# Kernel optimization log

Hardware: AMD Instinct MI355X
Metric: run time of the kernel (lower is better)

Reference implementation:

```python
import jax, jax.numpy as jnp
import numpy as np

B, I, H = 32768, 512, 512


def _uniform(key, shape, fan_in):
    bound = 1.0 / np.sqrt(fan_in)
    return jax.random.uniform(key, shape, jnp.float32, -bound, bound)


def setup_inputs() -> dict:
    key = jax.random.key(0)
    ks = jax.random.split(key, 16)
    inp = {
        "x": jax.random.normal(ks[0], (B, I), jnp.float32),
        "h": jax.random.normal(ks[1], (B, H), jnp.float32),
        "c_prev": jax.random.normal(ks[2], (B, H), jnp.float32),
        # weights stored as [in, out] so we apply x @ W (transpose of torch layout)
        "Wxi": _uniform(ks[3], (I, H), I), "bxi": _uniform(ks[4], (H,), I),
        "Whi": _uniform(ks[5], (H, H), H),
        "Wxf": _uniform(ks[6], (I, H), I), "bxf": _uniform(ks[7], (H,), I),
        "Whf": _uniform(ks[8], (H, H), H),
        "Wxc": _uniform(ks[9], (I, H), I), "bxc": _uniform(ks[10], (H,), I),
        "Whc": _uniform(ks[11], (H, H), H),
        "Wxo": _uniform(ks[12], (I, H), I), "bxo": _uniform(ks[13], (H,), I),
        "Who": _uniform(ks[14], (H, H), H),
    }
    return inp


def reference(x, h, c_prev, Wxi, bxi, Whi, Wxf, bxf, Whf, Wxc, bxc, Whc, Wxo, bxo, Who):
    # Faithful to source: peephole (w_c) projections are dead code; the
    # forget path f*c_prev is computed then discarded, so c_next = i * tanh(.)
    i = jax.nn.sigmoid(x @ Wxi + bxi + h @ Whi)            # input gate
    f = jax.nn.sigmoid(x @ Wxf + bxf + h @ Whf)            # computed, unused (as in source)
    c_next = i * jnp.tanh(x @ Wxc + bxc + h @ Whc)         # NOTE: no f*c_prev term (source bug)
    o = jax.nn.sigmoid(x @ Wxo + bxo + h @ Who)            # output gate
    h_next = o * jnp.tanh(c_next)
    del f, c_prev  # unused, matching the original module's effective math
    return (h_next, c_next)
```

## Files before the change

kernel.cpp:

```cpp
#include <hip/hip_runtime.h>
#include <hip/hip_bf16.h>


typedef unsigned short u16;
typedef u16 u16x8 __attribute__((ext_vector_type(8)));
typedef __bf16 bf16x8 __attribute__((ext_vector_type(8)));
typedef float f32x4 __attribute__((ext_vector_type(4)));

#define B_DIM 32768
#define H_DIM 512
#define K_DIM 1024
#define BH_ELEMS (B_DIM * H_DIM)
#define U_ELEMS ((long)B_DIM * K_DIM)
#define WT_BYTES ((size_t)(3u * 512u * 1024u * 2u))
#define U_BYTES ((size_t)U_ELEMS * 2u)

#define GLOBAL_AS(p) ((__attribute__((address_space(1))) void*)(p))
#define LDS_AS(p)    ((__attribute__((address_space(3))) void*)(p))

__device__ __forceinline__ float bf2f(u16 u) {
    unsigned v = ((unsigned)u) << 16;
    float f;
    __builtin_memcpy(&f, &v, 4);
    return f;
}

__device__ __forceinline__ u16 f2bf16u(float f) {
    __hip_bfloat16 b = __float2bfloat16(f);
    u16 u;
    __builtin_memcpy(&u, &b, 2);
    return u;
}

__device__ __forceinline__ float fast_rcp(float x) {
    return __builtin_amdgcn_rcpf(x);
}

__device__ __forceinline__ float fast_sigmoid(float x) {
    return fast_rcp(1.0f + __expf(-x));
}

__device__ __forceinline__ float fast_tanh(float x) {
    float e = __expf(-2.0f * fabsf(x));
    float r = (1.0f - e) * fast_rcp(1.0f + e);
    return x < 0.0f ? -r : r;
}

__device__ __forceinline__ bool derive_isbf(const unsigned* __restrict__ x, int tid) {
    const unsigned lo = x[tid & 63] & 0xFFFFu;
    const unsigned e = (lo >> 7) & 0xFFu;
    const bool sane = (e >= 100u && e <= 140u) || (lo == 0u);
    return __popcll(__ballot(sane)) >= 48;
}

__device__ __forceinline__ void gload16(const u16* g, u16* l) {
    __builtin_amdgcn_global_load_lds(GLOBAL_AS((u16*)g), LDS_AS(l), 16, 0, 0);
}

__global__ __launch_bounds__(256) void prep(
    const void* __restrict__ x, const void* __restrict__ h,
    const void* __restrict__ Wxi, const void* __restrict__ Whi,
    const void* __restrict__ Wxc, const void* __restrict__ Whc,
    const void* __restrict__ Wxo, const void* __restrict__ Who,
    u16* __restrict__ Wt, u16* __restrict__ U)
{
    __shared__ u16 tile[32][33];
    const int tid = threadIdx.x;
    const bool isbf = derive_isbf((const unsigned*)x, tid);
    const int bid = blockIdx.x;

    if (bid < 1536) {
        const int bz = bid >> 8, rem = bid & 255;
        const int by = rem >> 4, bx = rem & 15;
        const int g = bz >> 1, half = bz & 1;
        const void* src;
        if (g == 0)      src = half ? Whi : Wxi;
        else if (g == 1) src = half ? Whc : Wxc;
        else             src = half ? Who : Wxo;
        const int kk = by * 32, nn = bx * 32;
        const int tx = tid & 31, ty = tid >> 5;
        if (isbf) {
            const u16* s = (const u16*)src;
#pragma unroll
            for (int i2 = 0; i2 < 4; ++i2)
                tile[ty + 8 * i2][tx] = s[(kk + ty + 8 * i2) * 512 + nn + tx];
        } else {
            const float* s = (const float*)src;
#pragma unroll
            for (int i2 = 0; i2 < 4; ++i2)
                tile[ty + 8 * i2][tx] = f2bf16u(s[(kk + ty + 8 * i2) * 512 + nn + tx]);
        }
        __syncthreads();
#pragma unroll
        for (int i2 = 0; i2 < 4; ++i2)
            Wt[(long)g * 524288 + (long)(nn + ty + 8 * i2) * 1024 + half * 512 + kk + tx]
                = tile[tx][ty + 8 * i2];
    } else {
        const long stride = 4096L * 256L;
        for (long t = (long)(bid - 1536) * 256 + tid;
             t < (U_ELEMS >> 3); t += stride) {
            const long e = t << 3;
            const int r = (int)(e >> 10);
            const int k = (int)(e & 1023);
            const void* src = (k < 512) ? x : h;
            const long so = (long)r * 512 + (k & 511);
            u16x8 o;
            if (isbf) {
                o = *(const u16x8*)((const u16*)src + so);
            } else {
                const float* s = (const float*)src + so;
                f32x4 p0 = *(const f32x4*)s;
                f32x4 p1 = *(const f32x4*)(s + 4);
#pragma unroll
                for (int j = 0; j < 4; ++j) {
                    o[j] = f2bf16u(p0[j]);
                    o[4 + j] = f2bf16u(p1[j]);
                }
            }
            *(u16x8*)(U + e) = o;
        }
    }
}

__global__ __launch_bounds__(256, 2) void lstm_gemm_v3(
    const void* __restrict__ x,
    const u16* __restrict__ U, const u16* __restrict__ Wt,
    const void* __restrict__ bxi, const void* __restrict__ bxc,
    const void* __restrict__ bxo, void* __restrict__ out)
{
    __shared__ __align__(16) u16 As[2][128 * 64];
    __shared__ __align__(16) u16 Bs[2][3 * 64 * 64];

    const int tid    = threadIdx.x;
    const bool isbf  = derive_isbf((const unsigned*)x, tid);
    const int lane   = tid & 63;
    const int wave   = tid >> 6;
    const int wave_m = wave & 1;
    const int wave_n = wave >> 1;

    const int swz = (blockIdx.x & 7) * 256 + (blockIdx.x >> 3);
    const int m0 = (swz >> 3) * 128;
    const int n0 = (swz & 7) * 64;

    const int srow = lane >> 3;
    const int sk2  = (lane & 7) ^ srow;
    const u16* a_src[4];
#pragma unroll
    for (int j = 0; j < 4; ++j) {
        const int ca = wave * 4 + j;
        a_src[j] = U + (long)(m0 + ca * 8 + srow) * 1024 + sk2 * 8;
    }
    const u16* b_src[6];
#pragma unroll
    for (int q = 0; q < 6; ++q) {
        const int cb = q * 4 + wave;
        const int g = cb >> 3;
        const int nrow = (cb & 7) * 8 + srow;
        b_src[q] = Wt + (long)g * 524288 + (long)(n0 + nrow) * 1024 + sk2 * 8;
    }

#define STAGE_TILE(bi, kofs) do {                                         \
    _Pragma("unroll")                                                     \
    for (int j_ = 0; j_ < 4; ++j_)                                        \
        gload16(a_src[j_] + (kofs), &As[bi][(wave * 4 + j_) * 512]);      \
    _Pragma("unroll")                                                     \
    for (int q_ = 0; q_ < 6; ++q_)                                        \
        gload16(b_src[q_] + (kofs), &Bs[bi][(q_ * 4 + wave) * 512]);      \
} while (0)

    int a_off[4];
#pragma unroll
    for (int mt = 0; mt < 4; ++mt) {
        const int row = wave_m * 64 + mt * 16 + (lane & 15);
        const int p = (lane >> 4) ^ (row & 7);
        a_off[mt] = row * 64 + p * 8;
    }
    int b_off[3][2];
#pragma unroll
    for (int g = 0; g < 3; ++g)
#pragma unroll
        for (int nt = 0; nt < 2; ++nt) {
            const int row = wave_n * 32 + nt * 16 + (lane & 15);
            const int p = (lane >> 4) ^ (row & 7);
            b_off[g][nt] = g * 4096 + row * 64 + p * 8;
        }

    f32x4 acc[3][4][2];
    const f32x4 zero = {0.f, 0.f, 0.f, 0.f};
#pragma unroll
    for (int g = 0; g < 3; ++g)
#pragma unroll
        for (int mt = 0; mt < 4; ++mt)
#pragma unroll
            for (int nt = 0; nt < 2; ++nt)
                acc[g][mt][nt] = zero;

    STAGE_TILE(0, 0);
    __syncthreads();
#pragma unroll
    for (int t = 0; t < 16; ++t) {
        const int cur = t & 1;
        if (t < 15) STAGE_TILE(cur ^ 1, (t + 1) * 64);

#pragma unroll
        for (int kk = 0; kk < 2; ++kk) {
            const int kx = kk * 32;
            bf16x8 af[4];
#pragma unroll
            for (int mt = 0; mt < 4; ++mt)
                af[mt] = *(const bf16x8*)&As[cur][a_off[mt] ^ kx];
            bf16x8 bfr[3][2];
#pragma unroll
            for (int g = 0; g < 3; ++g)
#pragma unroll
                for (int nt = 0; nt < 2; ++nt)
                    bfr[g][nt] = *(const bf16x8*)&Bs[cur][b_off[g][nt] ^ kx];

#pragma unroll
            for (int g = 0; g < 3; ++g)
#pragma unroll
                for (int mt = 0; mt < 4; ++mt)
#pragma unroll
                    for (int nt = 0; nt < 2; ++nt)
                        acc[g][mt][nt] = __builtin_amdgcn_mfma_f32_16x16x32_bf16(
                            af[mt], bfr[g][nt], acc[g][mt][nt], 0, 0, 0);
        }
        if (t < 15) __syncthreads();
    }
#undef STAGE_TILE

    const int colbase = n0 + wave_n * 32 + (lane & 15);
    float bi[2], bc[2], bo[2];
#pragma unroll
    for (int nt = 0; nt < 2; ++nt) {
        const int col = colbase + nt * 16;
        if (isbf) {
            bi[nt] = bf2f(((const u16*)bxi)[col]);
            bc[nt] = bf2f(((const u16*)bxc)[col]);
            bo[nt] = bf2f(((const u16*)bxo)[col]);
        } else {
            bi[nt] = ((const float*)bxi)[col];
            bc[nt] = ((const float*)bxc)[col];
            bo[nt] = ((const float*)bxo)[col];
        }
    }

    const int rowbase = m0 + wave_m * 64 + (lane >> 4) * 4;
#pragma unroll
    for (int mt = 0; mt < 4; ++mt)
#pragma unroll
        for (int nt = 0; nt < 2; ++nt)
#pragma unroll
            for (int r = 0; r < 4; ++r) {
                const int row = rowbase + mt * 16 + r;
                const int col = colbase + nt * 16;
                const float iv = fast_sigmoid(acc[0][mt][nt][r] + bi[nt]);
                const float cv = iv * fast_tanh(acc[1][mt][nt][r] + bc[nt]);
                const float ov = fast_sigmoid(acc[2][mt][nt][r] + bo[nt]);
                const float hv = ov * fast_tanh(cv);
                const long idx = (long)row * 512 + col;
                if (isbf) {
                    ((u16*)out)[idx]            = f2bf16u(hv);
                    ((u16*)out)[BH_ELEMS + idx] = f2bf16u(cv);
                } else {
                    ((float*)out)[idx]            = hv;
                    ((float*)out)[BH_ELEMS + idx] = cv;
                }
            }
}

__global__ __launch_bounds__(256, 2) void lstm_gemm_fb(
    const void* __restrict__ x, const void* __restrict__ h,
    const u16* __restrict__ Wt,
    const void* __restrict__ bxi, const void* __restrict__ bxc,
    const void* __restrict__ bxo, void* __restrict__ out)
{
    __shared__ __align__(16) u16 As[128 * 32];
    __shared__ __align__(16) u16 Bs[3 * 64 * 32];

    const int tid    = threadIdx.x;
    const bool isbf  = derive_isbf((const unsigned*)x, tid);
    const int lane   = tid & 63;
    const int wave   = tid >> 6;
    const int wave_m = wave & 1;
    const int wave_n = wave >> 1;
    const int m0 = blockIdx.y * 128;
    const int n0 = blockIdx.x * 64;

    const int trow = tid >> 2, tkc = (tid & 3) * 8;
    const long a_g0 = (long)(m0 + trow)      * 512 + tkc;
    const long a_g1 = (long)(m0 + 64 + trow) * 512 + tkc;
    const int  a_l0 = tid * 8;
    const int  a_l1 = 2048 + tid * 8;
    long b_g[3];
#pragma unroll
    for (int q = 0; q < 3; ++q)
        b_g[q] = (long)q * 524288 + (long)(n0 + trow) * 1024 + tkc;

    int a_ld[4];
#pragma unroll
    for (int mt = 0; mt < 4; ++mt)
        a_ld[mt] = (wave_m * 64 + mt * 16 + (lane & 15)) * 32 + (lane >> 4) * 8;
    int b_ld[3][2];
#pragma unroll
    for (int g = 0; g < 3; ++g)
#pragma unroll
        for (int nt = 0; nt < 2; ++nt)
            b_ld[g][nt] = g * 2048 + (wave_n * 32 + nt * 16 + (lane & 15)) * 32 + (lane >> 4) * 8;

    f32x4 acc[3][4][2];
    const f32x4 zero = {0.f, 0.f, 0.f, 0.f};
#pragma unroll
    for (int g = 0; g < 3; ++g)
#pragma unroll
        for (int mt = 0; mt < 4; ++mt)
#pragma unroll
            for (int nt = 0; nt < 2; ++nt)
                acc[g][mt][nt] = zero;

    for (int k0 = 0; k0 < K_DIM; k0 += 32) {
        const void* src = (k0 < 512) ? x : h;
        const long kadj = (k0 < 512) ? k0 : (k0 - 512);

        bf16x8 av0, av1, bv[3];
        if (isbf) {
            const u16* s = (const u16*)src + kadj;
            u16x8 t0 = *(const u16x8*)(s + a_g0);
            u16x8 t1 = *(const u16x8*)(s + a_g1);
            __builtin_memcpy(&av0, &t0, 16);
            __builtin_memcpy(&av1, &t1, 16);
        } else {
            const float* s = (const float*)src + kadj;
            f32x4 p0 = *(const f32x4*)(s + a_g0);
            f32x4 p1 = *(const f32x4*)(s + a_g0 + 4);
            f32x4 q0 = *(const f32x4*)(s + a_g1);
            f32x4 q1 = *(const f32x4*)(s + a_g1 + 4);
#pragma unroll
            for (int j = 0; j < 4; ++j) {
                av0[j] = (__bf16)p0[j]; av0[4 + j] = (__bf16)p1[j];
                av1[j] = (__bf16)q0[j]; av1[4 + j] = (__bf16)q1[j];
            }
        }
#pragma unroll
        for (int q = 0; q < 3; ++q) {
            u16x8 t = *(const u16x8*)(Wt + b_g[q] + k0);
            __builtin_memcpy(&bv[q], &t, 16);
        }

        __syncthreads();
        *(bf16x8*)&As[a_l0] = av0;
        *(bf16x8*)&As[a_l1] = av1;
#pragma unroll
        for (int q = 0; q < 3; ++q)
            *(bf16x8*)&Bs[q * 2048 + tid * 8] = bv[q];
        __syncthreads();

        bf16x8 af[4];
#pragma unroll
        for (int mt = 0; mt < 4; ++mt)
            af[mt] = *(const bf16x8*)&As[a_ld[mt]];
        bf16x8 bfr[3][2];
#pragma unroll
        for (int g = 0; g < 3; ++g)
#pragma unroll
            for (int nt = 0; nt < 2; ++nt)
                bfr[g][nt] = *(const bf16x8*)&Bs[b_ld[g][nt]];

#pragma unroll
        for (int g = 0; g < 3; ++g)
#pragma unroll
            for (int mt = 0; mt < 4; ++mt)
#pragma unroll
            for (int nt = 0; nt < 2; ++nt)
                acc[g][mt][nt] = __builtin_amdgcn_mfma_f32_16x16x32_bf16(
                    af[mt], bfr[g][nt], acc[g][mt][nt], 0, 0, 0);
    }

    const int colbase = n0 + wave_n * 32 + (lane & 15);
    float bi[2], bc[2], bo[2];
#pragma unroll
    for (int nt = 0; nt < 2; ++nt) {
        const int col = colbase + nt * 16;
        if (isbf) {
            bi[nt] = bf2f(((const u16*)bxi)[col]);
            bc[nt] = bf2f(((const u16*)bxc)[col]);
            bo[nt] = bf2f(((const u16*)bxo)[col]);
        } else {
            bi[nt] = ((const float*)bxi)[col];
            bc[nt] = ((const float*)bxc)[col];
            bo[nt] = ((const float*)bxo)[col];
        }
    }

    const int rowbase = m0 + wave_m * 64 + (lane >> 4) * 4;
#pragma unroll
    for (int mt = 0; mt < 4; ++mt)
#pragma unroll
        for (int nt = 0; nt < 2; ++nt)
#pragma unroll
            for (int r = 0; r < 4; ++r) {
                const int row = rowbase + mt * 16 + r;
                const int col = colbase + nt * 16;
                const float iv = fast_sigmoid(acc[0][mt][nt][r] + bi[nt]);
                const float cv = iv * fast_tanh(acc[1][mt][nt][r] + bc[nt]);
                const float ov = fast_sigmoid(acc[2][mt][nt][r] + bo[nt]);
                const float hv = ov * fast_tanh(cv);
                const long idx = (long)row * 512 + col;
                if (isbf) {
                    ((u16*)out)[idx]            = f2bf16u(hv);
                    ((u16*)out)[BH_ELEMS + idx] = f2bf16u(cv);
                } else {
                    ((float*)out)[idx]            = hv;
                    ((float*)out)[BH_ELEMS + idx] = cv;
                }
            }
}

extern "C" void kernel_launch(void* const* d_in, const int* in_sizes, int n_in,
                              void* d_out, int out_size, void* d_ws, size_t ws_size,
                              hipStream_t stream) {
    const void* x   = d_in[0];
    const void* h   = d_in[1];
    const void* Wxi = d_in[3];
    const void* bxi = d_in[4];
    const void* Whi = d_in[5];
    const void* Wxc = d_in[9];
    const void* bxc = d_in[10];
    const void* Whc = d_in[11];
    const void* Wxo = d_in[12];
    const void* bxo = d_in[13];
    const void* Who = d_in[14];

    u16* Wt = (u16*)d_ws;
    const size_t need = WT_BYTES + U_BYTES;

    if (ws_size >= need) {
        u16* U = (u16*)((char*)d_ws + WT_BYTES);
        prep<<<dim3(1536 + 4096), dim3(256), 0, stream>>>(
            x, h, Wxi, Whi, Wxc, Whc, Wxo, Who, Wt, U);
        lstm_gemm_v3<<<dim3(2048), dim3(256), 0, stream>>>(
            x, U, Wt, bxi, bxc, bxo, d_out);
    } else {
        prep<<<dim3(1536), dim3(256), 0, stream>>>(
            x, h, Wxi, Whi, Wxc, Whc, Wxo, Who, Wt, nullptr);
        lstm_gemm_fb<<<dim3(8, 256), dim3(256), 0, stream>>>(
            x, h, Wt, bxi, bxc, bxo, d_out);
    }
}
```

Baseline: 380.6 us.

## Fuse x/h fp32-to-bf16 conversion into GEMM A-tile staging, drop U buffer

Removes the pre-pass that concatenated x and h into a bf16 U buffer in workspace. The GEMM now loads A tiles straight from x or h: fp32 data goes through registers, is converted to bf16 and written to swizzled LDS after the MFMA block, while bf16 inputs keep the direct global-to-LDS path. This avoids writing and re-reading a 64 MB intermediate. In exchange, each A tile is re-read in fp32 (twice the bytes) by every N-block, adds register pressure, and the loop unroll is reduced to 2.

```diff
diff --git a/kernel.cpp b/kernel.cpp
--- a/kernel.cpp
+++ b/kernel.cpp
@@ -11,9 +11,7 @@
 #define H_DIM 512
 #define K_DIM 1024
 #define BH_ELEMS (B_DIM * H_DIM)
-#define U_ELEMS ((long)B_DIM * K_DIM)
 #define WT_BYTES ((size_t)(3u * 512u * 1024u * 2u))
-#define U_BYTES ((size_t)U_ELEMS * 2u)
 
 #define GLOBAL_AS(p) ((__attribute__((address_space(1))) void*)(p))
 #define LDS_AS(p)    ((__attribute__((address_space(3))) void*)(p))
@@ -58,73 +56,47 @@
 }
 
 __global__ __launch_bounds__(256) void prep(
-    const void* __restrict__ x, const void* __restrict__ h,
+    const void* __restrict__ x,
     const void* __restrict__ Wxi, const void* __restrict__ Whi,
     const void* __restrict__ Wxc, const void* __restrict__ Whc,
     const void* __restrict__ Wxo, const void* __restrict__ Who,
-    u16* __restrict__ Wt, u16* __restrict__ U)
+    u16* __restrict__ Wt)
 {
     __shared__ u16 tile[32][33];
     const int tid = threadIdx.x;
     const bool isbf = derive_isbf((const unsigned*)x, tid);
     const int bid = blockIdx.x;
 
-    if (bid < 1536) {
-        const int bz = bid >> 8, rem = bid & 255;
-        const int by = rem >> 4, bx = rem & 15;
-        const int g = bz >> 1, half = bz & 1;
-        const void* src;
-        if (g == 0)      src = half ? Whi : Wxi;
-        else if (g == 1) src = half ? Whc : Wxc;
-        else             src = half ? Who : Wxo;
-        const int kk = by * 32, nn = bx * 32;
-        const int tx = tid & 31, ty = tid >> 5;
-        if (isbf) {
-            const u16* s = (const u16*)src;
-#pragma unroll
-            for (int i2 = 0; i2 < 4; ++i2)
-                tile[ty + 8 * i2][tx] = s[(kk + ty + 8 * i2) * 512 + nn + tx];
-        } else {
-            const float* s = (const float*)src;
-#pragma unroll
-            for (int i2 = 0; i2 < 4; ++i2)
-                tile[ty + 8 * i2][tx] = f2bf16u(s[(kk + ty + 8 * i2) * 512 + nn + tx]);
-        }
-        __syncthreads();
+    const int bz = bid >> 8, rem = bid & 255;
+    const int by = rem >> 4, bx = rem & 15;
+    const int g = bz >> 1, half = bz & 1;
+    const void* src;
+    if (g == 0)      src = half ? Whi : Wxi;
+    else if (g == 1) src = half ? Whc : Wxc;
+    else             src = half ? Who : Wxo;
+    const int kk = by * 32, nn = bx * 32;
+    const int tx = tid & 31, ty = tid >> 5;
+    if (isbf) {
+        const u16* s = (const u16*)src;
 #pragma unroll
         for (int i2 = 0; i2 < 4; ++i2)
-            Wt[(long)g * 524288 + (long)(nn + ty + 8 * i2) * 1024 + half * 512 + kk + tx]
-                = tile[tx][ty + 8 * i2];
+            tile[ty + 8 * i2][tx] = s[(kk + ty + 8 * i2) * 512 + nn + tx];
     } else {
-        const long stride = 4096L * 256L;
-        for (long t = (long)(bid - 1536) * 256 + tid;
-             t < (U_ELEMS >> 3); t += stride) {
-            const long e = t << 3;
-            const int r = (int)(e >> 10);
-            const int k = (int)(e & 1023);
-            const void* src = (k < 512) ? x : h;
-            const long so = (long)r * 512 + (k & 511);
-            u16x8 o;
-            if (isbf) {
-                o = *(const u16x8*)((const u16*)src + so);
-            } else {
-                const float* s = (const float*)src + so;
-                f32x4 p0 = *(const f32x4*)s;
-                f32x4 p1 = *(const f32x4*)(s + 4);
-#pragma unroll
-                for (int j = 0; j < 4; ++j) {
-                    o[j] = f2bf16u(p0[j]);
-                    o[4 + j] = f2bf16u(p1[j]);
-                }
-            }
-            *(u16x8*)(U + e) = o;
-        }
-    }
-}
-
-__global__ __launch_bounds__(256, 2) void lstm_gemm_v3(
-    const void* __restrict__ x,
-    const u16* __restrict__ U, const u16* __restrict__ Wt,
+        const float* s = (const float*)src;
+#pragma unroll
+        for (int i2 = 0; i2 < 4; ++i2)
+            tile[ty + 8 * i2][tx] = f2bf16u(s[(kk + ty + 8 * i2) * 512 + nn + tx]);
+    }
+    __syncthreads();
+#pragma unroll
+    for (int i2 = 0; i2 < 4; ++i2)
+        Wt[(long)g * 524288 + (long)(nn + ty + 8 * i2) * 1024 + half * 512 + kk + tx]
+            = tile[tx][ty + 8 * i2];
+}
+
+__global__ __launch_bounds__(256, 2) void lstm_gemm_v4(
+    const void* __restrict__ x, const void* __restrict__ h,
+    const u16* __restrict__ Wt,
     const void* __restrict__ bxi, const void* __restrict__ bxc,
     const void* __restrict__ bxo, void* __restrict__ out)
 {
@@ -144,12 +116,6 @@
 
     const int srow = lane >> 3;
     const int sk2  = (lane & 7) ^ srow;
-    const u16* a_src[4];
-#pragma unroll
-    for (int j = 0; j < 4; ++j) {
-        const int ca = wave * 4 + j;
-        a_src[j] = U + (long)(m0 + ca * 8 + srow) * 1024 + sk2 * 8;
-    }
     const u16* b_src[6];
 #pragma unroll
     for (int q = 0; q < 6; ++q) {
@@ -158,16 +124,52 @@
         const int nrow = (cb & 7) * 8 + srow;
         b_src[q] = Wt + (long)g * 524288 + (long)(n0 + nrow) * 1024 + sk2 * 8;
     }
-
-#define STAGE_TILE(bi, kofs) do {                                         \
-    _Pragma("unroll")                                                     \
-    for (int j_ = 0; j_ < 4; ++j_)                                        \
-        gload16(a_src[j_] + (kofs), &As[bi][(wave * 4 + j_) * 512]);      \
+    long a_goff[4];
+#pragma unroll
+    for (int j = 0; j < 4; ++j) {
+        const int trow = (wave * 4 + j) * 8 + srow;
+        a_goff[j] = (long)(m0 + trow) * 512 + sk2 * 8;
+    }
+    const int arow  = tid >> 3;
+    const int ac8   = tid & 7;
+    const int aslot = (ac8 ^ (arow & 7)) * 8;
+
+#define STAGE_B(bi, kofs) do {                                            \
     _Pragma("unroll")                                                     \
     for (int q_ = 0; q_ < 6; ++q_)                                        \
         gload16(b_src[q_] + (kofs), &Bs[bi][(q_ * 4 + wave) * 512]);      \
 } while (0)
 
+#define STAGE_A_BF(bi, srcp, koff) do {                                   \
+    _Pragma("unroll")                                                     \
+    for (int j_ = 0; j_ < 4; ++j_)                                        \
+        gload16((const u16*)(srcp) + a_goff[j_] + (koff),                 \
+                &As[bi][(wave * 4 + j_) * 512]);                          \
+} while (0)
+
+#define A_LOAD_F32(srcp, koff) do {                                       \
+    _Pragma("unroll")                                                     \
+    for (int j_ = 0; j_ < 4; ++j_) {                                      \
+        const float* p_ = (const float*)(srcp)                            \
+            + (long)(m0 + arow + 32 * j_) * 512 + (koff) + ac8 * 8;       \
+        alo[j_] = *(const f32x4*)p_;                                      \
+        ahi[j_] = *(const f32x4*)(p_ + 4);                                \
+    }                                                                     \
+} while (0)
+
+#define A_CVT_WRITE(bi) do {                                              \
+    _Pragma("unroll")                                                     \
+    for (int j_ = 0; j_ < 4; ++j_) {                                      \
+        bf16x8 v_;                                                        \
+        _Pragma("unroll")                                                 \
+        for (int e_ = 0; e_ < 4; ++e_) {                                  \
+            v_[e_]     = (__bf16)alo[j_][e_];                             \
+            v_[4 + e_] = (__bf16)ahi[j_][e_];                             \
+        }                                                                 \
+        *(bf16x8*)&As[bi][(arow + 32 * j_) * 64 + aslot] = v_;            \
+    }                                                                     \
+} while (0)
+
     int a_off[4];
 #pragma unroll
     for (int mt = 0; mt < 4; ++mt) {
@@ -195,12 +197,29 @@
             for (int nt = 0; nt < 2; ++nt)
                 acc[g][mt][nt] = zero;
 
-    STAGE_TILE(0, 0);
+    f32x4 alo[4], ahi[4];
+
+    if (isbf) {
+        STAGE_A_BF(0, x, 0);
+    } else {
+        A_LOAD_F32(x, 0);
+    }
+    STAGE_B(0, 0);
+    if (!isbf) A_CVT_WRITE(0);
     __syncthreads();
-#pragma unroll
+
+#pragma unroll 2
     for (int t = 0; t < 16; ++t) {
         const int cur = t & 1;
-        if (t < 15) STAGE_TILE(cur ^ 1, (t + 1) * 64);
+        const int nxt = cur ^ 1;
+        if (t < 15) {
+            const int kb = (t + 1) * 64;
+            const void* srcp = (kb < 512) ? x : h;
+            const int koff = kb & 511;
+            if (isbf) STAGE_A_BF(nxt, srcp, koff);
+            else      A_LOAD_F32(srcp, koff);
+            STAGE_B(nxt, kb);
+        }
 
 #pragma unroll
         for (int kk = 0; kk < 2; ++kk) {
@@ -225,9 +244,15 @@
                         acc[g][mt][nt] = __builtin_amdgcn_mfma_f32_16x16x32_bf16(
                             af[mt], bfr[g][nt], acc[g][mt][nt], 0, 0, 0);
         }
-        if (t < 15) __syncthreads();
-    }
-#undef STAGE_TILE
+        if (t < 15) {
+            if (!isbf) A_CVT_WRITE(nxt);
+            __syncthreads();
+        }
+    }
+#undef STAGE_B
+#undef STAGE_A_BF
+#undef A_LOAD_F32
+#undef A_CVT_WRITE
 
     const int colbase = n0 + wave_n * 32 + (lane & 15);
     float bi[2], bc[2], bo[2];
@@ -432,17 +457,14 @@
     const void* Who = d_in[14];
 
     u16* Wt = (u16*)d_ws;
-    const size_t need = WT_BYTES + U_BYTES;
-
-    if (ws_size >= need) {
-        u16* U = (u16*)((char*)d_ws + WT_BYTES);
-        prep<<<dim3(1536 + 4096), dim3(256), 0, stream>>>(
-            x, h, Wxi, Whi, Wxc, Whc, Wxo, Who, Wt, U);
-        lstm_gemm_v3<<<dim3(2048), dim3(256), 0, stream>>>(
-            x, U, Wt, bxi, bxc, bxo, d_out);
+
+    prep<<<dim3(1536), dim3(256), 0, stream>>>(
+        x, Wxi, Whi, Wxc, Whc, Wxo, Who, Wt);
+
+    if (ws_size >= WT_BYTES) {
+        lstm_gemm_v4<<<dim3(2048), dim3(256), 0, stream>>>(
+            x, h, Wt, bxi, bxc, bxo, d_out);
     } else {
-        prep<<<dim3(1536), dim3(256), 0, stream>>>(
-            x, h, Wxi, Whi, Wxc, Whc, Wxo, Who, Wt, nullptr);
         lstm_gemm_fb<<<dim3(8, 256), dim3(256), 0, stream>>>(
             x, h, Wt, bxi, bxc, bxo, d_out);
     }
```

New measurement: 406.9 us. 1.07x slower.

## Replace GEMM kernel with 512-thread 128x128 tile and fine-grained phased pipeline

Applied to the files above, without the earlier changes.

Replaces the 256-thread 128x64-tile GEMM with a 512-thread (8-wave) kernel computing 128x128 output tiles per block, halving the block count. The K loop is split into half-tile phases, each with its own barrier and explicit vmcnt waits, so global-to-LDS loads for upcoming K slices overlap with MFMA work. It also raises wave priority around the MFMA bursts and uses an XCD-aware block-to-tile mapping. The aim is better reuse of A and B tiles and hidden memory latency, traded against more barriers, occupancy of one block per CU, and hand-tuned waitcnt counts that are fragile.

```diff
diff --git a/kernel.cpp b/kernel.cpp
--- a/kernel.cpp
+++ b/kernel.cpp
@@ -122,14 +122,183 @@
     }
 }
 
-__global__ __launch_bounds__(256, 2) void lstm_gemm_v3(
+__global__ __launch_bounds__(512, 1) void lstm_gemm_v5(
     const void* __restrict__ x,
     const u16* __restrict__ U, const u16* __restrict__ Wt,
     const void* __restrict__ bxi, const void* __restrict__ bxc,
     const void* __restrict__ bxo, void* __restrict__ out)
 {
-    __shared__ __align__(16) u16 As[2][128 * 64];
-    __shared__ __align__(16) u16 Bs[2][3 * 64 * 64];
+    __shared__ __align__(16) u16 Al[4 * 4096];
+    __shared__ __align__(16) u16 Bl[4 * 12288];
+
+    const int tid  = threadIdx.x;
+    const bool isbf = derive_isbf((const unsigned*)x, tid);
+    const int lane = tid & 63;
+    const int wave = tid >> 6;
+    const int wave_m = wave >> 2;
+    const int wave_n = wave & 3;
+
+    const int bid = blockIdx.x;
+    const int xcd = bid & 7, ii = bid >> 3;
+    const int m0 = (xcd * 32 + (ii >> 2)) * 128;
+    const int n0 = (ii & 3) * 128;
+
+    const int arow = tid >> 2;
+    const int asrc = (((tid & 3) ^ ((arow >> 1) & 3))) * 8;
+    const long a_base = (long)(m0 + arow) * 1024 + asrc;
+    long b_base[3];
+#pragma unroll
+    for (int g = 0; g < 3; ++g)
+        b_base[g] = (long)(g * 512 + n0 + arow) * 1024 + asrc;
+
+    int arof[4];
+#pragma unroll
+    for (int mr = 0; mr < 4; ++mr) {
+        const int row = wave_m * 64 + mr * 16 + (lane & 15);
+        const int slot = (lane >> 4) ^ ((row >> 1) & 3);
+        arof[mr] = row * 32 + slot * 8;
+    }
+    int brof[3][2];
+#pragma unroll
+    for (int g = 0; g < 3; ++g)
+#pragma unroll
+        for (int nr = 0; nr < 2; ++nr) {
+            const int row = wave_n * 32 + nr * 16 + (lane & 15);
+            const int slot = (lane >> 4) ^ ((row >> 1) & 3);
+            brof[g][nr] = g * 4096 + row * 32 + slot * 8;
+        }
+
+    f32x4 acc[3][4][2];
+    const f32x4 zero = {0.f, 0.f, 0.f, 0.f};
+#pragma unroll
+    for (int g = 0; g < 3; ++g)
+#pragma unroll
+        for (int mr = 0; mr < 4; ++mr)
+#pragma unroll
+            for (int nr = 0; nr < 2; ++nr)
+                acc[g][mr][nr] = zero;
+
+    bf16x8 bfr[3][2];
+
+#define SA(BUF, KH, KOFF) \
+    gload16(U + a_base + (KOFF) + (KH) * 32, &Al[((BUF) * 2 + (KH)) * 4096 + wave * 512])
+#define SB(BUF, KH, KOFF) do {                                                \
+    _Pragma("unroll")                                                         \
+    for (int g_ = 0; g_ < 3; ++g_)                                            \
+        gload16(Wt + b_base[g_] + (KOFF) + (KH) * 32,                         \
+                &Bl[((BUF) * 2 + (KH)) * 12288 + g_ * 4096 + wave * 512]);    \
+} while (0)
+#define NOSTAGE ((void)0)
+#define VMW(N) asm volatile("s_waitcnt vmcnt(" #N ")" ::: "memory")
+#define BAR() __builtin_amdgcn_s_barrier()
+
+#define PH(BUF, KK, MH, STAGE) do {                                           \
+    bf16x8 af0 = *(const bf16x8*)&Al[((BUF)*2+(KK))*4096 + arof[(MH)*2+0]];   \
+    bf16x8 af1 = *(const bf16x8*)&Al[((BUF)*2+(KK))*4096 + arof[(MH)*2+1]];   \
+    if ((MH) == 0) {                                                          \
+        _Pragma("unroll")                                                     \
+        for (int g_ = 0; g_ < 3; ++g_)                                        \
+            _Pragma("unroll")                                                 \
+            for (int nr_ = 0; nr_ < 2; ++nr_)                                 \
+                bfr[g_][nr_] = *(const bf16x8*)&Bl[((BUF)*2+(KK))*12288 + brof[g_][nr_]]; \
+    }                                                                         \
+    STAGE;                                                                    \
+    BAR();                                                                    \
+    asm volatile("s_waitcnt lgkmcnt(0)" ::: "memory");                        \
+    __builtin_amdgcn_sched_barrier(0);                                        \
+    __builtin_amdgcn_s_setprio(1);                                            \
+    _Pragma("unroll")                                                         \
+    for (int g_ = 0; g_ < 3; ++g_)                                            \
+        _Pragma("unroll")                                                     \
+        for (int nr_ = 0; nr_ < 2; ++nr_) {                                   \
+            acc[g_][(MH)*2+0][nr_] = __builtin_amdgcn_mfma_f32_16x16x32_bf16( \
+                af0, bfr[g_][nr_], acc[g_][(MH)*2+0][nr_], 0, 0, 0);          \
+            acc[g_][(MH)*2+1][nr_] = __builtin_amdgcn_mfma_f32_16x16x32_bf16( \
+                af1, bfr[g_][nr_], acc[g_][(MH)*2+1][nr_], 0, 0, 0);          \
+        }                                                                     \
+    __builtin_amdgcn_s_setprio(0);                                            \
+} while (0)
+
+    SA(0, 0, 0); SA(0, 1, 0); SB(0, 0, 0); SB(0, 1, 0);
+    SB(1, 0, 64); SA(1, 0, 64); SB(1, 1, 64);
+    VMW(7);
+    BAR();
+
+    for (int t = 0; t < 7; ++t) {
+        const int kb = t * 128;
+        PH(0, 0, 0, SA(1, 1, kb + 64));            BAR();
+        PH(0, 0, 1, SB(0, 0, kb + 128));           BAR();
+        PH(0, 1, 0, SA(0, 0, kb + 128));           BAR();
+        PH(0, 1, 1, SB(0, 1, kb + 128)); VMW(7);   BAR();
+        PH(1, 0, 0, SA(0, 1, kb + 128));           BAR();
+        PH(1, 0, 1, SB(1, 0, kb + 192));           BAR();
+        PH(1, 1, 0, SA(1, 0, kb + 192));           BAR();
+        PH(1, 1, 1, SB(1, 1, kb + 192)); VMW(7);   BAR();
+    }
+    PH(0, 0, 0, SA(1, 1, 960));  BAR();
+    PH(0, 0, 1, NOSTAGE);        BAR();
+    PH(0, 1, 0, NOSTAGE);        BAR();
+    PH(0, 1, 1, NOSTAGE); VMW(0); BAR();
+    PH(1, 0, 0, NOSTAGE);        BAR();
+    PH(1, 0, 1, NOSTAGE);        BAR();
+    PH(1, 1, 0, NOSTAGE);        BAR();
+    PH(1, 1, 1, NOSTAGE);
+
+#undef SA
+#undef SB
+#undef NOSTAGE
+#undef VMW
+#undef BAR
+#undef PH
+
+    const int colbase = n0 + wave_n * 32 + (lane & 15);
+    float bi[2], bc[2], bo[2];
+#pragma unroll
+    for (int nr = 0; nr < 2; ++nr) {
+        const int col = colbase + nr * 16;
+        if (isbf) {
+            bi[nr] = bf2f(((const u16*)bxi)[col]);
+            bc[nr] = bf2f(((const u16*)bxc)[col]);
+            bo[nr] = bf2f(((const u16*)bxo)[col]);
+        } else {
+            bi[nr] = ((const float*)bxi)[col];
+            bc[nr] = ((const float*)bxc)[col];
+            bo[nr] = ((const float*)bxo)[col];
+        }
+    }
+
+    const int rowbase = m0 + wave_m * 64 + (lane >> 4) * 4;
+#pragma unroll
+    for (int mr = 0; mr < 4; ++mr)
+#pragma unroll
+        for (int nr = 0; nr < 2; ++nr)
+#pragma unroll
+            for (int r = 0; r < 4; ++r) {
+                const int row = rowbase + mr * 16 + r;
+                const int col = colbase + nr * 16;
+                const float iv = fast_sigmoid(acc[0][mr][nr][r] + bi[nr]);
+                const float cv = iv * fast_tanh(acc[1][mr][nr][r] + bc[nr]);
+                const float ov = fast_sigmoid(acc[2][mr][nr][r] + bo[nr]);
+                const float hv = ov * fast_tanh(cv);
+                const long idx = (long)row * 512 + col;
+                if (isbf) {
+                    ((u16*)out)[idx]            = f2bf16u(hv);
+                    ((u16*)out)[BH_ELEMS + idx] = f2bf16u(cv);
+                } else {
+                    ((float*)out)[idx]            = hv;
+                    ((float*)out)[BH_ELEMS + idx] = cv;
+                }
+            }
+}
+
+__global__ __launch_bounds__(256, 2) void lstm_gemm_fb(
+    const void* __restrict__ x, const void* __restrict__ h,
+    const u16* __restrict__ Wt,
+    const void* __restrict__ bxi, const void* __restrict__ bxc,
+    const void* __restrict__ bxo, void* __restrict__ out)
+{
+    __shared__ __align__(16) u16 As[128 * 32];
+    __shared__ __align__(16) u16 Bs[3 * 64 * 32];
 
     const int tid    = threadIdx.x;
     const bool isbf  = derive_isbf((const unsigned*)x, tid);
@@ -137,53 +306,29 @@
     const int wave   = tid >> 6;
     const int wave_m = wave & 1;
     const int wave_n = wave >> 1;
-
-    const int swz = (blockIdx.x & 7) * 256 + (blockIdx.x >> 3);
-    const int m0 = (swz >> 3) * 128;
-    const int n0 = (swz & 7) * 64;
-
-    const int srow = lane >> 3;
-    const int sk2  = (lane & 7) ^ srow;
-    const u16* a_src[4];
-#pragma unroll
-    for (int j = 0; j < 4; ++j) {
-        const int ca = wave * 4 + j;
-        a_src[j] = U + (long)(m0 + ca * 8 + srow) * 1024 + sk2 * 8;
-    }
-    const u16* b_src[6];
-#pragma unroll
-    for (int q = 0; q < 6; ++q) {
-        const int cb = q * 4 + wave;
-        const int g = cb >> 3;
-        const int nrow = (cb & 7) * 8 + srow;
-        b_src[q] = Wt + (long)g * 524288 + (long)(n0 + nrow) * 1024 + sk2 * 8;
-    }
-
-#define STAGE_TILE(bi, kofs) do {                                         \
-    _Pragma("unroll")                                                     \
-    for (int j_ = 0; j_ < 4; ++j_)                                        \
-        gload16(a_src[j_] + (kofs), &As[bi][(wave * 4 + j_) * 512]);      \
-    _Pragma("unroll")                                                     \
-    for (int q_ = 0; q_ < 6; ++q_)                                        \
-        gload16(b_src[q_] + (kofs), &Bs[bi][(q_ * 4 + wave) * 512]);      \
-} while (0)
-
-    int a_off[4];
-#pragma unroll
-    for (int mt = 0; mt < 4; ++mt) {
-        const int row = wave_m * 64 + mt * 16 + (lane & 15);
-        const int p = (lane >> 4) ^ (row & 7);
-        a_off[mt] = row * 64 + p * 8;
-    }
-    int b_off[3][2];
+    const int m0 = blockIdx.y * 128;
+    const int n0 = blockIdx.x * 64;
+
+    const int trow = tid >> 2, tkc = (tid & 3) * 8;
+    const long a_g0 = (long)(m0 + trow)      * 512 + tkc;
+    const long a_g1 = (long)(m0 + 64 + trow) * 512 + tkc;
+    const int  a_l0 = tid * 8;
+    const int  a_l1 = 2048 + tid * 8;
+    long b_g[3];
+#pragma unroll
+    for (int q = 0; q < 3; ++q)
+        b_g[q] = (long)q * 524288 + (long)(n0 + trow) * 1024 + tkc;
+
+    int a_ld[4];
+#pragma unroll
+    for (int mt = 0; mt < 4; ++mt)
+        a_ld[mt] = (wave_m * 64 + mt * 16 + (lane & 15)) * 32 + (lane >> 4) * 8;
+    int b_ld[3][2];
 #pragma unroll
     for (int g = 0; g < 3; ++g)
 #pragma unroll
-        for (int nt = 0; nt < 2; ++nt) {
-            const int row = wave_n * 32 + nt * 16 + (lane & 15);
-            const int p = (lane >> 4) ^ (row & 7);
-            b_off[g][nt] = g * 4096 + row * 64 + p * 8;
-        }
+        for (int nt = 0; nt < 2; ++nt)
+            b_ld[g][nt] = g * 2048 + (wave_n * 32 + nt * 16 + (lane & 15)) * 32 + (lane >> 4) * 8;
 
     f32x4 acc[3][4][2];
     const f32x4 zero = {0.f, 0.f, 0.f, 0.f};
@@ -195,39 +340,63 @@
             for (int nt = 0; nt < 2; ++nt)
                 acc[g][mt][nt] = zero;
 
-    STAGE_TILE(0, 0);
-    __syncthreads();
-#pragma unroll
-    for (int t = 0; t < 16; ++t) {
-        const int cur = t & 1;
-        if (t < 15) STAGE_TILE(cur ^ 1, (t + 1) * 64);
-
-#pragma unroll
-        for (int kk = 0; kk < 2; ++kk) {
-            const int kx = kk * 32;
-            bf16x8 af[4];
+    for (int k0 = 0; k0 < K_DIM; k0 += 32) {
+        const void* src = (k0 < 512) ? x : h;
+        const long kadj = (k0 < 512) ? k0 : (k0 - 512);
+
+        bf16x8 av0, av1, bv[3];
+        if (isbf) {
+            const u16* s = (const u16*)src + kadj;
+            u16x8 t0 = *(const u16x8*)(s + a_g0);
+            u16x8 t1 = *(const u16x8*)(s + a_g1);
+            __builtin_memcpy(&av0, &t0, 16);
+            __builtin_memcpy(&av1, &t1, 16);
+        } else {
+            const float* s = (const float*)src + kadj;
+            f32x4 p0 = *(const f32x4*)(s + a_g0);
+            f32x4 p1 = *(const f32x4*)(s + a_g0 + 4);
+            f32x4 q0 = *(const f32x4*)(s + a_g1);
+            f32x4 q1 = *(const f32x4*)(s + a_g1 + 4);
+#pragma unroll
+            for (int j = 0; j < 4; ++j) {
+                av0[j] = (__bf16)p0[j]; av0[4 + j] = (__bf16)p1[j];
+                av1[j] = (__bf16)q0[j]; av1[4 + j] = (__bf16)q1[j];
+            }
+        }
+#pragma unroll
+        for (int q = 0; q < 3; ++q) {
+            u16x8 t = *(const u16x8*)(Wt + b_g[q] + k0);
+            __builtin_memcpy(&bv[q], &t, 16);
+        }
+
+        __syncthreads();
+        *(bf16x8*)&As[a_l0] = av0;
+        *(bf16x8*)&As[a_l1] = av1;
+#pragma unroll
+        for (int q = 0; q < 3; ++q)
+            *(bf16x8*)&Bs[q * 2048 + tid * 8] = bv[q];
+        __syncthreads();
+
+        bf16x8 af[4];
+#pragma unroll
+        for (int mt = 0; mt < 4; ++mt)
+            af[mt] = *(const bf16x8*)&As[a_ld[mt]];
+        bf16x8 bfr[3][2];
+#pragma unroll
+        for (int g = 0; g < 3; ++g)
+#pragma unroll
+            for (int nt = 0; nt < 2; ++nt)
+                bfr[g][nt] = *(const bf16x8*)&Bs[b_ld[g][nt]];
+
+#pragma unroll
+        for (int g = 0; g < 3; ++g)
 #pragma unroll
             for (int mt = 0; mt < 4; ++mt)
-                af[mt] = *(const bf16x8*)&As[cur][a_off[mt] ^ kx];
-            bf16x8 bfr[3][2];
-#pragma unroll
-            for (int g = 0; g < 3; ++g)
-#pragma unroll
-                for (int nt = 0; nt < 2; ++nt)
-                    bfr[g][nt] = *(const bf16x8*)&Bs[cur][b_off[g][nt] ^ kx];
-
-#pragma unroll
-            for (int g = 0; g < 3; ++g)
-#pragma unroll
-                for (int mt = 0; mt < 4; ++mt)
-#pragma unroll
-                    for (int nt = 0; nt < 2; ++nt)
-                        acc[g][mt][nt] = __builtin_amdgcn_mfma_f32_16x16x32_bf16(
-                            af[mt], bfr[g][nt], acc[g][mt][nt], 0, 0, 0);
-        }
-        if (t < 15) __syncthreads();
-    }
-#undef STAGE_TILE
+#pragma unroll
+            for (int nt = 0; nt < 2; ++nt)
+                acc[g][mt][nt] = __builtin_amdgcn_mfma_f32_16x16x32_bf16(
+                    af[mt], bfr[g][nt], acc[g][mt][nt], 0, 0, 0);
+    }
 
     const int colbase = n0 + wave_n * 32 + (lane & 15);
     float bi[2], bc[2], bo[2];
@@ -269,153 +438,6 @@
             }
 }
 
-__global__ __launch_bounds__(256, 2) void lstm_gemm_fb(
-    const void* __restrict__ x, const void* __restrict__ h,
-    const u16* __restrict__ Wt,
-    const void* __restrict__ bxi, const void* __restrict__ bxc,
-    const void* __restrict__ bxo, void* __restrict__ out)
-{
-    __shared__ __align__(16) u16 As[128 * 32];
-    __shared__ __align__(16) u16 Bs[3 * 64 * 32];
-
-    const int tid    = threadIdx.x;
-    const bool isbf  = derive_isbf((const unsigned*)x, tid);
-    const int lane   = tid & 63;
-    const int wave   = tid >> 6;
-    const int wave_m = wave & 1;
-    const int wave_n = wave >> 1;
-    const int m0 = blockIdx.y * 128;
-    const int n0 = blockIdx.x * 64;
-
-    const int trow = tid >> 2, tkc = (tid & 3) * 8;
-    const long a_g0 = (long)(m0 + trow)      * 512 + tkc;
-    const long a_g1 = (long)(m0 + 64 + trow) * 512 + tkc;
-    const int  a_l0 = tid * 8;
-    const int  a_l1 = 2048 + tid * 8;
-    long b_g[3];
-#pragma unroll
-    for (int q = 0; q < 3; ++q)
-        b_g[q] = (long)q * 524288 + (long)(n0 + trow) * 1024 + tkc;
-
-    int a_ld[4];
-#pragma unroll
-    for (int mt = 0; mt < 4; ++mt)
-        a_ld[mt] = (wave_m * 64 + mt * 16 + (lane & 15)) * 32 + (lane >> 4) * 8;
-    int b_ld[3][2];
-#pragma unroll
-    for (int g = 0; g < 3; ++g)
-#pragma unroll
-        for (int nt = 0; nt < 2; ++nt)
-            b_ld[g][nt] = g * 2048 + (wave_n * 32 + nt * 16 + (lane & 15)) * 32 + (lane >> 4) * 8;
-
-    f32x4 acc[3][4][2];
-    const f32x4 zero = {0.f, 0.f, 0.f, 0.f};
-#pragma unroll
-    for (int g = 0; g < 3; ++g)
-#pragma unroll
-        for (int mt = 0; mt < 4; ++mt)
-#pragma unroll
-            for (int nt = 0; nt < 2; ++nt)
-                acc[g][mt][nt] = zero;
-
-    for (int k0 = 0; k0 < K_DIM; k0 += 32) {
-        const void* src = (k0 < 512) ? x : h;
-        const long kadj = (k0 < 512) ? k0 : (k0 - 512);
-
-        bf16x8 av0, av1, bv[3];
-        if (isbf) {
-            const u16* s = (const u16*)src + kadj;
-            u16x8 t0 = *(const u16x8*)(s + a_g0);
-            u16x8 t1 = *(const u16x8*)(s + a_g1);
-            __builtin_memcpy(&av0, &t0, 16);
-            __builtin_memcpy(&av1, &t1, 16);
-        } else {
-            const float* s = (const float*)src + kadj;
-            f32x4 p0 = *(const f32x4*)(s + a_g0);
-            f32x4 p1 = *(const f32x4*)(s + a_g0 + 4);
-            f32x4 q0 = *(const f32x4*)(s + a_g1);
-            f32x4 q1 = *(const f32x4*)(s + a_g1 + 4);
-#pragma unroll
-            for (int j = 0; j < 4; ++j) {
-                av0[j] = (__bf16)p0[j]; av0[4 + j] = (__bf16)p1[j];
-                av1[j] = (__bf16)q0[j]; av1[4 + j] = (__bf16)q1[j];
-            }
-        }
-#pragma unroll
-        for (int q = 0; q < 3; ++q) {
-            u16x8 t = *(const u16x8*)(Wt + b_g[q] + k0);
-            __builtin_memcpy(&bv[q], &t, 16);
-        }
-
-        __syncthreads();
-        *(bf16x8*)&As[a_l0] = av0;
-        *(bf16x8*)&As[a_l1] = av1;
-#pragma unroll
-        for (int q = 0; q < 3; ++q)
-            *(bf16x8*)&Bs[q * 2048 + tid * 8] = bv[q];
-        __syncthreads();
-
-        bf16x8 af[4];
-#pragma unroll
-        for (int mt = 0; mt < 4; ++mt)
-            af[mt] = *(const bf16x8*)&As[a_ld[mt]];
-        bf16x8 bfr[3][2];
-#pragma unroll
-        for (int g = 0; g < 3; ++g)
-#pragma unroll
-            for (int nt = 0; nt < 2; ++nt)
-                bfr[g][nt] = *(const bf16x8*)&Bs[b_ld[g][nt]];
-
-#pragma unroll
-        for (int g = 0; g < 3; ++g)
-#pragma unroll
-            for (int mt = 0; mt < 4; ++mt)
-#pragma unroll
-            for (int nt = 0; nt < 2; ++nt)
-                acc[g][mt][nt] = __builtin_amdgcn_mfma_f32_16x16x32_bf16(
-                    af[mt], bfr[g][nt], acc[g][mt][nt], 0, 0, 0);
-    }
-
-    const int colbase = n0 + wave_n * 32 + (lane & 15);
-    float bi[2], bc[2], bo[2];
-#pragma unroll
-    for (int nt = 0; nt < 2; ++nt) {
-        const int col = colbase + nt * 16;
-        if (isbf) {
-            bi[nt] = bf2f(((const u16*)bxi)[col]);
-            bc[nt] = bf2f(((const u16*)bxc)[col]);
-            bo[nt] = bf2f(((const u16*)bxo)[col]);
-        } else {
-            bi[nt] = ((const float*)bxi)[col];
-            bc[nt] = ((const float*)bxc)[col];
-            bo[nt] = ((const float*)bxo)[col];
-        }
-    }
-
-    const int rowbase = m0 + wave_m * 64 + (lane >> 4) * 4;
-#pragma unroll
-    for (int mt = 0; mt < 4; ++mt)
-#pragma unroll
-        for (int nt = 0; nt < 2; ++nt)
-#pragma unroll
-            for (int r = 0; r < 4; ++r) {
-                const int row = rowbase + mt * 16 + r;
-                const int col = colbase + nt * 16;
-                const float iv = fast_sigmoid(acc[0][mt][nt][r] + bi[nt]);
-                const float cv = iv * fast_tanh(acc[1][mt][nt][r] + bc[nt]);
-                const float ov = fast_sigmoid(acc[2][mt][nt][r] + bo[nt]);
-                const float hv = ov * fast_tanh(cv);
-                const long idx = (long)row * 512 + col;
-                if (isbf) {
-                    ((u16*)out)[idx]            = f2bf16u(hv);
-                    ((u16*)out)[BH_ELEMS + idx] = f2bf16u(cv);
-                } else {
-                    ((float*)out)[idx]            = hv;
-                    ((float*)out)[BH_ELEMS + idx] = cv;
-                }
-            }
-}
-
 extern "C" void kernel_launch(void* const* d_in, const int* in_sizes, int n_in,
                               void* d_out, int out_size, void* d_ws, size_t ws_size,
                               hipStream_t stream) {
@@ -438,7 +460,7 @@
         u16* U = (u16*)((char*)d_ws + WT_BYTES);
         prep<<<dim3(1536 + 4096), dim3(256), 0, stream>>>(
             x, h, Wxi, Whi, Wxc, Whc, Wxo, Who, Wt, U);
-        lstm_gemm_v3<<<dim3(2048), dim3(256), 0, stream>>>(
+        lstm_gemm_v5<<<dim3(1024), dim3(512), 0, stream>>>(
             x, U, Wt, bxi, bxc, bxo, d_out);
     } else {
         prep<<<dim3(1536), dim3(256), 0, stream>>>(
```

Measured after the change: 411.9 us. +8.2%, slower.
